# Kernel optimization log

Measured on AMD Instinct MI355X. Metric: run time of the kernel, lower is better.

Reference implementation:

```python
import jax, jax.numpy as jnp
import numpy as np

NUM_FORMULAS = 1024
INPUT_DIM = 256
BATCH = 2048


def setup_inputs() -> dict:
    key = jax.random.key(0)
    k_x, k_mu, k_sigma = jax.random.split(key, 3)
    inputs = jax.random.normal(k_x, (BATCH, INPUT_DIM), dtype=jnp.float32)
    # keras random_normal initializer default stddev = 0.05
    mu = 0.05 * jax.random.normal(k_mu, (NUM_FORMULAS, INPUT_DIM), dtype=jnp.float32)
    sigma = 0.05 * jax.random.normal(k_sigma, (1, NUM_FORMULAS, INPUT_DIM), dtype=jnp.float32)
    temperature = jnp.float32(2.0)
    return {"inputs": inputs, "mu": mu, "sigma": sigma, "temperature": temperature}


def reference(inputs, mu, sigma, temperature):
    # diff: (batch, num_formulas, dim)
    diff = inputs[:, None, :] - mu[None, :, :]
    # weighted L2 norm over feature dim -> (batch, num_formulas)
    dist = jnp.sqrt(jnp.sum(jnp.square(diff * sigma), axis=-1))
    loc = jnp.exp(-dist)
    # sigmoid-gated temperature, softmax over formulas (last axis)
    return jax.nn.softmax(jax.nn.sigmoid(temperature) * loc, axis=-1)
```

## Files before the change

kernel.cpp:

```cpp
#include <hip/hip_runtime.h>
#include <math.h>

#define NF 1024
#define DIM 256
#define BATCH 2048
#define K 512
#define BMF 16
#define KS 32
#define NSTEP (K / KS)

#define WS_C_OFF (NF * K * 2)

typedef __attribute__((ext_vector_type(8))) short short8;
typedef __attribute__((ext_vector_type(4))) float f32x4;

__device__ __forceinline__ unsigned short f2bf(float f) {
    unsigned u = __float_as_uint(f);
    u += 0x7fffu + ((u >> 16) & 1u);
    return (unsigned short)(u >> 16);
}

__global__ __launch_bounds__(256) void k_prep(const float* __restrict__ mu,
                                              const float* __restrict__ sigma,
                                              uint4* __restrict__ Bb4,
                                              float* __restrict__ c) {
    const int t = threadIdx.x;
    const int f = blockIdx.x * 4 + (t >> 6);
    const int sq = t & 63;
    const float4 mv = *(const float4*)&mu[f * DIM + sq * 4];
    const float4 sv = *(const float4*)&sigma[f * DIM + sq * 4];

    uint4 pk; float cp = 0.f;
    {
        const float s2x = sv.x * sv.x;
        pk.x = (unsigned)f2bf(s2x) | ((unsigned)f2bf(-2.0f * s2x * mv.x) << 16);
        cp += s2x * mv.x * mv.x;
        const float s2y = sv.y * sv.y;
        pk.y = (unsigned)f2bf(s2y) | ((unsigned)f2bf(-2.0f * s2y * mv.y) << 16);
        cp += s2y * mv.y * mv.y;
        const float s2z = sv.z * sv.z;
        pk.z = (unsigned)f2bf(s2z) | ((unsigned)f2bf(-2.0f * s2z * mv.z) << 16);
        cp += s2z * mv.z * mv.z;
        const float s2w = sv.w * sv.w;
        pk.w = (unsigned)f2bf(s2w) | ((unsigned)f2bf(-2.0f * s2w * mv.w) << 16);
        cp += s2w * mv.w * mv.w;
    }
    Bb4[(sq >> 2) * 4096 + (sq & 3) * 1024 + f] = pk;

    #pragma unroll
    for (int off = 32; off > 0; off >>= 1) cp += __shfl_down(cp, off, 64);
    if ((t & 63) == 0) c[f] = cp;
}

__global__ __launch_bounds__(1024, 1) void k_fused(const float* __restrict__ x,
                                                   const ushort* __restrict__ Bb,
                                                   const float* __restrict__ c,
                                                   const float* __restrict__ temp,
                                                   float* __restrict__ out) {
    const int t = threadIdx.x;
    const int w = t >> 6;
    const int lane = t & 63;
    const int m16 = lane & 15;
    const int q = lane >> 4;
    const int r0 = blockIdx.x * BMF;

    __shared__ __align__(16) ushort ldsA[BMF * K];
    __shared__ float wsum[16][BMF];
    __shared__ float rowInv[BMF];

    {
        const int row = t >> 6, kc = t & 63;
        const float4 v = *(const float4*)&x[(r0 + row) * DIM + kc * 4];
        uint4 pk;
        pk.x = (unsigned)f2bf(v.x * v.x) | ((unsigned)f2bf(v.x) << 16);
        pk.y = (unsigned)f2bf(v.y * v.y) | ((unsigned)f2bf(v.y) << 16);
        pk.z = (unsigned)f2bf(v.z * v.z) | ((unsigned)f2bf(v.z) << 16);
        pk.w = (unsigned)f2bf(v.w * v.w) | ((unsigned)f2bf(v.w) << 16);
        *(uint4*)&ldsA[(row * 64 + (kc ^ (row & 7))) * 8] = pk;
    }

    f32x4 acc[4];
    #pragma unroll
    for (int ct = 0; ct < 4; ++ct) acc[ct] = (f32x4){0.f, 0.f, 0.f, 0.f};

    const ushort* bp = Bb + q * (NF * 8) + (w * 64 + m16) * 8;

#define BLOAD(dst, s)                                                       \
    _Pragma("unroll")                                                       \
    for (int ct = 0; ct < 4; ++ct)                                          \
        dst[ct] = *(const short8*)(bp + (s) * (NF * KS) + ct * 128);

#define BCOMP(src, s)                                                       \
    {                                                                       \
        const int kcq = (s) * 4 + q;                                        \
        const short8 av =                                                   \
            *(const short8*)&ldsA[(m16 * 64 + (kcq ^ (m16 & 7))) * 8];      \
        _Pragma("unroll")                                                   \
        for (int ct = 0; ct < 4; ++ct)                                      \
            acc[ct] = __builtin_amdgcn_mfma_f32_16x16x32_bf16(              \
                av, src[ct], acc[ct], 0, 0, 0);                             \
    }

    short8 bA[4], bB[4], bC[4], bD[4];
    BLOAD(bA, 0) BLOAD(bB, 1) BLOAD(bC, 2) BLOAD(bD, 3)

    __syncthreads();

    #pragma unroll 1
    for (int g = 0; g < 3; ++g) {
        const int s = g * 4;
        BCOMP(bA, s)     BLOAD(bA, s + 4)
        BCOMP(bB, s + 1) BLOAD(bB, s + 5)
        BCOMP(bC, s + 2) BLOAD(bC, s + 6)
        BCOMP(bD, s + 3) BLOAD(bD, s + 7)
    }
    BCOMP(bA, 12) BCOMP(bB, 13) BCOMP(bC, 14) BCOMP(bD, 15)

#undef BLOAD
#undef BCOMP

    const float g = 1.0f / (1.0f + __expf(-temp[0]));
    float s4[4] = {0.f, 0.f, 0.f, 0.f};
    #pragma unroll
    for (int ct = 0; ct < 4; ++ct) {
        const float cn = c[w * 64 + ct * 16 + m16];
        #pragma unroll
        for (int i = 0; i < 4; ++i) {
            const float dist2 = acc[ct][i] + cn;
            const float dist = sqrtf(fmaxf(dist2, 0.0f));
            const float p = __expf(g * __expf(-dist));
            acc[ct][i] = p;
            s4[i] += p;
        }
    }
    #pragma unroll
    for (int i = 0; i < 4; ++i) {
        #pragma unroll
        for (int mask = 1; mask < 16; mask <<= 1)
            s4[i] += __shfl_xor(s4[i], mask, 64);
    }
    if (m16 == 0) {
        #pragma unroll
        for (int i = 0; i < 4; ++i) wsum[w][q * 4 + i] = s4[i];
    }
    __syncthreads();
    if (t < BMF) {
        float ssum = 0.f;
        #pragma unroll
        for (int ww = 0; ww < 16; ++ww) ssum += wsum[ww][t];
        rowInv[t] = 1.0f / ssum;
    }
    __syncthreads();

    float inv[4];
    #pragma unroll
    for (int i = 0; i < 4; ++i) inv[i] = rowInv[q * 4 + i];
    #pragma unroll
    for (int ct = 0; ct < 4; ++ct) {
        const int fcol = w * 64 + ct * 16 + m16;
        #pragma unroll
        for (int i = 0; i < 4; ++i)
            out[(r0 + q * 4 + i) * NF + fcol] = acc[ct][i] * inv[i];
    }
}

extern "C" void kernel_launch(void* const* d_in, const int* in_sizes, int n_in,
                              void* d_out, int out_size, void* d_ws, size_t ws_size,
                              hipStream_t stream) {
    const float* x     = (const float*)d_in[0];
    const float* mu    = (const float*)d_in[1];
    const float* sigma = (const float*)d_in[2];
    const float* temp  = (const float*)d_in[3];
    float* out = (float*)d_out;

    char* ws = (char*)d_ws;
    ushort* Bb = (ushort*)ws;
    float*  c  = (float*)(ws + WS_C_OFF);

    k_prep<<<NF / 4, 256, 0, stream>>>(mu, sigma, (uint4*)Bb, c);
    k_fused<<<BATCH / BMF, 1024, 0, stream>>>(x, Bb, c, temp, out);
}
```

Baseline: 75.90 us.

## Stream B operand through LDS via global_load_lds with double buffering

Replaces the register-held four-stage prefetch of B fragments with direct global-to-LDS loads (global_load_lds) into a per-wave double buffer, with explicit vmcnt waits and sched barriers. The aim is to free VGPRs and overlap the loads with the MFMA work. In exchange it adds an LDS round trip per B fragment, 128KB of LDS, and shallower prefetch depth (2 stages instead of 4), which may expose memory latency.

Measured after the change: 78.76 us. +3.8%, slower.

```diff
diff --git a/kernel.cpp b/kernel.cpp
--- a/kernel.cpp
+++ b/kernel.cpp
@@ -18,6 +18,12 @@
     unsigned u = __float_as_uint(f);
     u += 0x7fffu + ((u >> 16) & 1u);
     return (unsigned short)(u >> 16);
+}
+
+__device__ __forceinline__ void gl_lds16(const ushort* g, ushort* l) {
+    __builtin_amdgcn_global_load_lds(
+        (const __attribute__((address_space(1))) void*)g,
+        (__attribute__((address_space(3))) void*)l, 16, 0, 0);
 }
 
 __global__ __launch_bounds__(256) void k_prep(const float* __restrict__ mu,
@@ -65,6 +71,7 @@
     const int r0 = blockIdx.x * BMF;
 
     __shared__ __align__(16) ushort ldsA[BMF * K];
+    __shared__ __align__(16) ushort ldsB[16 * 2 * 2048];
     __shared__ float wsum[16][BMF];
     __shared__ float rowInv[BMF];
 
@@ -84,39 +91,54 @@
     for (int ct = 0; ct < 4; ++ct) acc[ct] = (f32x4){0.f, 0.f, 0.f, 0.f};
 
     const ushort* bp = Bb + q * (NF * 8) + (w * 64 + m16) * 8;
-
-#define BLOAD(dst, s)                                                       \
+    ushort* myB = &ldsB[w * 4096];
+
+#define ISSUE(sv, bufb)                                                     \
     _Pragma("unroll")                                                       \
     for (int ct = 0; ct < 4; ++ct)                                          \
-        dst[ct] = *(const short8*)(bp + (s) * (NF * KS) + ct * 128);
-
-#define BCOMP(src, s)                                                       \
+        gl_lds16(bp + (sv) * (NF * KS) + ct * 128,                          \
+                 myB + (bufb) * 2048 + ct * 512);
+
+#define BCOMP(sv, bufb)                                                     \
     {                                                                       \
-        const int kcq = (s) * 4 + q;                                        \
+        const int kcq = (sv) * 4 + q;                                       \
         const short8 av =                                                   \
             *(const short8*)&ldsA[(m16 * 64 + (kcq ^ (m16 & 7))) * 8];      \
         _Pragma("unroll")                                                   \
-        for (int ct = 0; ct < 4; ++ct)                                      \
+        for (int ct = 0; ct < 4; ++ct) {                                    \
+            const short8 bv = *(const short8*)&myB[(bufb) * 2048 +          \
+                                                   ct * 512 + lane * 8];    \
             acc[ct] = __builtin_amdgcn_mfma_f32_16x16x32_bf16(              \
-                av, src[ct], acc[ct], 0, 0, 0);                             \
-    }
-
-    short8 bA[4], bB[4], bC[4], bD[4];
-    BLOAD(bA, 0) BLOAD(bB, 1) BLOAD(bC, 2) BLOAD(bD, 3)
+                av, bv, acc[ct], 0, 0, 0);                                  \
+        }                                                                   \
+    }
 
     __syncthreads();
 
+    ISSUE(0, 0) ISSUE(1, 1)
+
     #pragma unroll 1
-    for (int g = 0; g < 3; ++g) {
-        const int s = g * 4;
-        BCOMP(bA, s)     BLOAD(bA, s + 4)
-        BCOMP(bB, s + 1) BLOAD(bB, s + 5)
-        BCOMP(bC, s + 2) BLOAD(bC, s + 6)
-        BCOMP(bD, s + 3) BLOAD(bD, s + 7)
-    }
-    BCOMP(bA, 12) BCOMP(bB, 13) BCOMP(bC, 14) BCOMP(bD, 15)
-
-#undef BLOAD
+    for (int g = 0; g < 7; ++g) {
+        const int s = g * 2;
+        asm volatile("s_waitcnt vmcnt(4)" ::: "memory");
+        __builtin_amdgcn_sched_barrier(0);
+        BCOMP(s, 0)
+        __builtin_amdgcn_sched_barrier(0);
+        ISSUE(s + 2, 0)
+        asm volatile("s_waitcnt vmcnt(4)" ::: "memory");
+        __builtin_amdgcn_sched_barrier(0);
+        BCOMP(s + 1, 1)
+        __builtin_amdgcn_sched_barrier(0);
+        ISSUE(s + 3, 1)
+    }
+    asm volatile("s_waitcnt vmcnt(4)" ::: "memory");
+    __builtin_amdgcn_sched_barrier(0);
+    BCOMP(14, 0)
+    asm volatile("s_waitcnt vmcnt(0)" ::: "memory");
+    __builtin_amdgcn_sched_barrier(0);
+    BCOMP(15, 1)
+
+#undef ISSUE
 #undef BCOMP
 
     const float g = 1.0f / (1.0f + __expf(-temp[0]));
```
